# Kernel optimization log

Measured on AMD Instinct MI355X. Metric: run time of the kernel, lower is better.

The kernel has to match this reference:

```python
import jax, jax.numpy as jnp
import numpy as np

GRID = 14  # encoded_image_size

def _grid_edge_index():
    # Exact replica of build_adjacency_matrix().nonzero(): 8-neighbor 14x14 grid.
    edges = []
    for r in range(GRID):
        for c in range(GRID):
            i = r * GRID + c
            for rr in range(max(0, r - 1), min(r + 2, GRID)):
                for cc in range(max(0, c - 1), min(c + 2, GRID)):
                    if rr == r and cc == c:
                        continue
                    edges.append((i, rr * GRID + cc))
    return np.asarray(edges, dtype=np.int64).T  # (2, 1404)


def setup_inputs() -> dict:
    key = jax.random.key(0)
    k1, k2, k3 = jax.random.split(key, 3)
    B, H, W, C, Hid = 128, 14, 14, 2048, 1024
    x = jax.random.normal(k1, (B, H, W, C), dtype=jnp.float32)
    edge_index = jnp.asarray(_grid_edge_index())
    W1 = jax.random.normal(k2, (C, Hid), dtype=jnp.float32) * (1.0 / np.sqrt(C))
    b1 = jnp.zeros((Hid,), jnp.float32)
    W2 = jax.random.normal(k3, (Hid, C), dtype=jnp.float32) * (1.0 / np.sqrt(Hid))
    b2 = jnp.zeros((C,), jnp.float32)
    return {"x": x, "edge_index": edge_index, "W1": W1, "b1": b1, "W2": W2, "b2": b2}


def _gcn_conv(h, W, b, src, dst, dinv):
    # PyG GCNConv: linear transform, symmetric deg-normalized (A+I) aggregation, bias.
    h = h @ W  # [N, out]
    norm = (dinv[src] * dinv[dst])[:, None]
    agg = jax.ops.segment_sum(h[src] * norm, dst, num_segments=h.shape[0])
    agg = agg + h * (dinv * dinv)[:, None]  # self-loop term, norm = 1/deg_i
    return agg + b


def reference(x, edge_index, W1, b1, W2, b2):
    B, H, Wd, C = x.shape
    N = B * H * Wd
    # Faithful to original: permute(0,3,1,2) then reshape(-1, C) (layout-scrambling).
    xf = jnp.transpose(x, (0, 3, 1, 2)).reshape(-1, C)  # [N, C]
    src, dst = edge_index[0], edge_index[1]
    # Degrees over ALL N nodes: self-loop (=1) everywhere + incoming grid edges
    # (only first 196 nodes have grid neighbors; rest are passthrough).
    deg = jnp.ones((N,), xf.dtype).at[dst].add(1.0)
    dinv = jax.lax.rsqrt(deg)
    h = jax.nn.relu(_gcn_conv(xf, W1, b1, src, dst, dinv))
    h = jax.nn.relu(_gcn_conv(h, W2, b2, src, dst, dinv))
    # reshape + permute(0,3,1,2) + permute(0,2,3,1) == identity back to NHWC.
    return h.reshape(B, H, Wd, C)
```

## Files before the change

### kernel.cpp

```cpp
#include <hip/hip_runtime.h>

typedef float  float4_t __attribute__((ext_vector_type(4)));
typedef __bf16 bf16x8   __attribute__((ext_vector_type(8)));

#define BM 256
#define BN 128
#define BK 64

#define GLD16(g, l)                                                        \
    __builtin_amdgcn_global_load_lds(                                      \
        (const __attribute__((address_space(1))) void*)(g),                \
        (__attribute__((address_space(3))) void*)(l), 16, 0, 0)

__global__ __launch_bounds__(256)
void transpose_x_kernel(const float* __restrict__ x, __bf16* __restrict__ A1)
{
    __shared__ float sm[32 * 221];
    const int b  = blockIdx.y;
    const int c0 = blockIdx.x * 32;
    const int t  = threadIdx.x;

    const float* xb = x + (size_t)b * 401408;
    const int c4 = (t & 7) * 4;
    const int p0 = t >> 3;
#pragma unroll
    for (int k = 0; k < 7; ++k) {
        int p = p0 + k * 32;
        if (p < 196) {
            float4_t v = *(const float4_t*)&xb[(size_t)p * 2048 + c0 + c4];
#pragma unroll
            for (int i = 0; i < 4; ++i)
                sm[(c4 + i) * 221 + p + (p >> 3)] = v[i];
        }
    }
    __syncthreads();

    __bf16* ab = A1 + (size_t)b * 401408 + (size_t)c0 * 196;
#pragma unroll
    for (int k = 0; k < 4; ++k) {
        int o8 = k * 256 + t;
        if (o8 < 784) {
            int o  = o8 * 8;
            int cc = o / 196;
            int pp = o - cc * 196;
            bf16x8 v;
#pragma unroll
            for (int i = 0; i < 8; ++i) {
                v[i] = (__bf16)sm[cc * 221 + pp + (pp >> 3)];
                if (++pp == 196) { pp = 0; ++cc; }
            }
            *(bf16x8*)(ab + o) = v;
        }
    }
}

__global__ void transpose_w_kernel(const float* __restrict__ W, __bf16* __restrict__ Wt,
                                   int K, int N)
{
    __shared__ float tile[32][33];
    const int kt = blockIdx.x * 32, nt = blockIdx.y * 32;
    const int tx = threadIdx.x, ty = threadIdx.y;
#pragma unroll
    for (int rr = 0; rr < 4; ++rr)
        tile[ty + rr * 8][tx] = W[(size_t)(kt + ty + rr * 8) * N + nt + tx];
    __syncthreads();
#pragma unroll
    for (int rr = 0; rr < 4; ++rr)
        Wt[(size_t)(nt + ty + rr * 8) * K + kt + tx] = (__bf16)tile[tx][ty + rr * 8];
}

template<bool OUT_BF16, int LNX>
__global__ __launch_bounds__(512, 2)
void gemm_bt_kernel(const __bf16* __restrict__ A,
                    const __bf16* __restrict__ Bt,
                    const float* __restrict__ bias,
                    void* __restrict__ out,
                    float* __restrict__ raw_out,
                    int M, int N, int K)
{
    __shared__ __bf16 lds[3 * 24576];

    const int tid  = threadIdx.x;
    const int wid  = tid >> 6;
    const int lane = tid & 63;

    const int lid  = blockIdx.x + gridDim.x * blockIdx.y;
    const int xcd  = lid & 7;
    const int i0   = lid >> 3;
    const int ni   = i0 & ((1 << LNX) - 1);
    const int mseq = i0 >> LNX;
    const int mi   = (mseq << 3) + xcd;
    const int row0 = mi * BM;
    if (row0 >= M) return;
    const int col0 = ni * BN;

    const int wave_m = (wid >> 1) * 64;
    const int wave_n = (wid & 1) * 64;

    float4_t acc[4][4];
#pragma unroll
    for (int i = 0; i < 4; ++i)
#pragma unroll
        for (int j = 0; j < 4; ++j)
            acc[i][j] = (float4_t){0.f, 0.f, 0.f, 0.f};

    const int    srow  = (wid << 3) + (lane >> 3);
    const int    scol  = ((lane & 7) ^ (lane >> 3)) << 3;
    const int    wb    = wid << 9;
    const __bf16* gA   = A  + (size_t)(row0 + srow) * K + scol;
    const __bf16* gB   = Bt + (size_t)(col0 + srow) * K + scol;
    const size_t rstep = (size_t)64 * K;

#define STAGE_P1(t, da) do {                                   \
    const __bf16* ga = gA + (size_t)(t) * BK;                  \
    GLD16(ga,             (da) +         wb);                  \
    GLD16(ga +     rstep, (da) + 4096  + wb);                  \
    GLD16(ga + 2 * rstep, (da) + 8192  + wb);                  \
} while (0)
#define STAGE_P2(t, da) do {                                   \
    const __bf16* ga = gA + (size_t)(t) * BK + 3 * rstep;      \
    const __bf16* gb = gB + (size_t)(t) * BK;                  \
    GLD16(ga,             (da) + 12288 + wb);                  \
    GLD16(gb,             (da) + 16384 + wb);                  \
    GLD16(gb +     rstep, (da) + 20480 + wb);                  \
} while (0)

    STAGE_P1(0, lds);         STAGE_P2(0, lds);
    STAGE_P1(1, lds + 24576); STAGE_P2(1, lds + 24576);
    asm volatile("s_waitcnt vmcnt(6)" ::: "memory");
    __builtin_amdgcn_s_barrier();
    __builtin_amdgcn_sched_barrier(0);

    const int xorv = lane & 7;
    const int kq   = lane >> 4;
    const int swz0 = (kq ^ xorv) << 3;
    const int arow = (wave_m + (lane & 15)) * 64;
    const int brow = (wave_n + (lane & 15)) * 64;

    const int NTt = K / BK;
    int cur = 0, st2 = 2;
    for (int t = 0; t < NTt; ++t) {
        const __bf16* cA = lds + cur * 24576;
        const __bf16* cB = cA + 16384;
        __bf16* dst2 = lds + st2 * 24576;
        const bool do_stage = (t < NTt - 2);

        bf16x8 bfr[2][4], af0[2][2];
#pragma unroll
        for (int x = 0; x < 2; ++x) {
            const int sz = swz0 ^ (x << 5);
#pragma unroll
            for (int j = 0; j < 4; ++j)
                bfr[x][j] = *(const bf16x8*)&cB[brow + j * 1024 + sz];
#pragma unroll
            for (int i = 0; i < 2; ++i)
                af0[x][i] = *(const bf16x8*)&cA[arow + i * 1024 + sz];
        }
        if (do_stage) STAGE_P1(t + 2, dst2);
        __builtin_amdgcn_s_barrier();
        __builtin_amdgcn_sched_barrier(0);
        __builtin_amdgcn_s_setprio(1);
#pragma unroll
        for (int x = 0; x < 2; ++x)
#pragma unroll
            for (int i = 0; i < 2; ++i)
#pragma unroll
                for (int j = 0; j < 4; ++j)
                    acc[i][j] = __builtin_amdgcn_mfma_f32_16x16x32_bf16(
                        af0[x][i], bfr[x][j], acc[i][j], 0, 0, 0);
        __builtin_amdgcn_s_setprio(0);

        bf16x8 af1[2][2];
#pragma unroll
        for (int x = 0; x < 2; ++x) {
            const int sz = swz0 ^ (x << 5);
#pragma unroll
            for (int i = 0; i < 2; ++i)
                af1[x][i] = *(const bf16x8*)&cA[arow + (i + 2) * 1024 + sz];
        }
        if (do_stage) STAGE_P2(t + 2, dst2);
        if (t < NTt - 1) {
            asm volatile("s_waitcnt lgkmcnt(0)" ::: "memory");
            if (do_stage) asm volatile("s_waitcnt vmcnt(6)" ::: "memory");
            else          asm volatile("s_waitcnt vmcnt(0)" ::: "memory");
            __builtin_amdgcn_s_barrier();
            __builtin_amdgcn_sched_barrier(0);
        }
        __builtin_amdgcn_s_setprio(1);
#pragma unroll
        for (int x = 0; x < 2; ++x)
#pragma unroll
            for (int i = 0; i < 2; ++i)
#pragma unroll
                for (int j = 0; j < 4; ++j)
                    acc[i + 2][j] = __builtin_amdgcn_mfma_f32_16x16x32_bf16(
                        af1[x][i], bfr[x][j], acc[i + 2][j], 0, 0, 0);
        __builtin_amdgcn_s_setprio(0);

        cur = (cur == 2) ? 0 : cur + 1;
        st2 = (st2 == 2) ? 0 : st2 + 1;
    }
#undef STAGE_P1
#undef STAGE_P2

    const int crow = (lane >> 4) * 4;
    const int ccol = lane & 15;
    const bool has_raw = (row0 == 0);
#pragma unroll
    for (int i = 0; i < 4; ++i) {
#pragma unroll
        for (int j = 0; j < 4; ++j) {
            int gcol = col0 + wave_n + j * 16 + ccol;
            float bv = bias[gcol];
#pragma unroll
            for (int r = 0; r < 4; ++r) {
                int grow = row0 + wave_m + i * 16 + crow + r;
                float v = acc[i][j][r];
                if (has_raw && grow < 196) raw_out[grow * N + gcol] = v;
                float o = fmaxf(v + bv, 0.f);
                if (OUT_BF16) ((__bf16*)out)[(size_t)grow * N + gcol] = (__bf16)o;
                else          ((float*)out)[(size_t)grow * N + gcol] = o;
            }
        }
    }
}

template<typename OutT>
__global__ void fixup_kernel(const float* __restrict__ raw, const float* __restrict__ bias,
                             OutT* __restrict__ out, int N)
{
    const int q = blockIdx.x;
    const int r = q / 14, c = q % 14;
    int nbr[8];
    int cnt = 0;
    for (int rr = (r > 0 ? r - 1 : 0); rr <= (r < 13 ? r + 1 : 13); ++rr)
        for (int cc = (c > 0 ? c - 1 : 0); cc <= (c < 13 ? c + 1 : 13); ++cc)
            if (!(rr == r && cc == c)) nbr[cnt++] = rr * 14 + cc;
    const float dq    = 1.f / sqrtf(1.f + (float)cnt);
    const float wself = 1.f / (1.f + (float)cnt);
    float wn[8];
    for (int t = 0; t < cnt; ++t) {
        int pr = nbr[t] / 14, pc = nbr[t] % 14;
        int pcnt = ((pr < 13 ? pr + 1 : 13) - (pr > 0 ? pr - 1 : 0) + 1) *
                   ((pc < 13 ? pc + 1 : 13) - (pc > 0 ? pc - 1 : 0) + 1) - 1;
        wn[t] = dq / sqrtf(1.f + (float)pcnt);
    }
    const int ch = blockIdx.y * 256 + threadIdx.x;
    float s = raw[q * N + ch] * wself;
    for (int t = 0; t < cnt; ++t) s += raw[nbr[t] * N + ch] * wn[t];
    float o = fmaxf(s + bias[ch], 0.f);
    out[(size_t)q * N + ch] = (OutT)o;
}

extern "C" void kernel_launch(void* const* d_in, const int* in_sizes, int n_in,
                              void* d_out, int out_size, void* d_ws, size_t ws_size,
                              hipStream_t stream)
{
    const float* x  = (const float*)d_in[0];
    const float* W1 = (const float*)d_in[2];
    const float* b1 = (const float*)d_in[3];
    const float* W2 = (const float*)d_in[4];
    const float* b2 = (const float*)d_in[5];

    const int M = 25088, C = 2048, Hid = 1024;

    __bf16* A1 = (__bf16*)d_out;

    char* ws = (char*)d_ws;
    __bf16* A2    = (__bf16*)(ws);
    __bf16* W1t   = (__bf16*)(ws + 51380224);
    __bf16* W2t   = (__bf16*)(ws + 55574528);
    float*  h1raw = (float*)(ws + 59768832);
    float*  h2raw = (float*)(ws + 60571648);

    transpose_x_kernel<<<dim3(64, 128), 256, 0, stream>>>(x, A1);
    transpose_w_kernel<<<dim3(C / 32, Hid / 32), dim3(32, 8), 0, stream>>>(W1, W1t, C, Hid);
    transpose_w_kernel<<<dim3(Hid / 32, C / 32), dim3(32, 8), 0, stream>>>(W2, W2t, Hid, C);

    gemm_bt_kernel<true, 3><<<dim3(Hid / BN, 104), 512, 0, stream>>>(
        A1, W1t, b1, (void*)A2, h1raw, M, Hid, C);
    fixup_kernel<__bf16><<<dim3(196, Hid / 256), 256, 0, stream>>>(h1raw, b1, A2, Hid);

    gemm_bt_kernel<false, 4><<<dim3(C / BN, 104), 512, 0, stream>>>(
        A2, W2t, b2, d_out, h2raw, M, C, Hid);
    fixup_kernel<float><<<dim3(196, C / 256), 256, 0, stream>>>(h2raw, b2, (float*)d_out, C);
}
```

Baseline: 634.6 us.

## Use 4-wave GEMM blocks with 128x64 per-wave tiles and BK=32

The GEMM block shrinks from 8 waves to 4, so each wave now computes a 128x64 output tile with 32 accumulators, and the K step drops to 32 with a new LDS swizzle and staging layout. The aim is more MFMA work per LDS fragment load and less LDS traffic per FLOP, plus one barrier per K step instead of two. In exchange, register pressure roughly doubles, the halved K step means twice as many loop iterations and syncs, and each block has fewer waves to hide latency.

```diff
diff --git a/kernel.cpp b/kernel.cpp
--- a/kernel.cpp
+++ b/kernel.cpp
@@ -5,7 +5,7 @@
 
 #define BM 256
 #define BN 128
-#define BK 64
+#define BK 32
 
 #define GLD16(g, l)                                                        \
     __builtin_amdgcn_global_load_lds(                                      \
@@ -70,7 +70,7 @@
 }
 
 template<bool OUT_BF16, int LNX>
-__global__ __launch_bounds__(512, 2)
+__global__ __launch_bounds__(256, 2)
 void gemm_bt_kernel(const __bf16* __restrict__ A,
                     const __bf16* __restrict__ Bt,
                     const float* __restrict__ bias,
@@ -78,7 +78,7 @@
                     float* __restrict__ raw_out,
                     int M, int N, int K)
 {
-    __shared__ __bf16 lds[3 * 24576];
+    __shared__ __bf16 lds[3 * 12288];
 
     const int tid  = threadIdx.x;
     const int wid  = tid >> 6;
@@ -94,91 +94,69 @@
     if (row0 >= M) return;
     const int col0 = ni * BN;
 
-    const int wave_m = (wid >> 1) * 64;
+    const int wave_m = (wid >> 1) * 128;
     const int wave_n = (wid & 1) * 64;
 
-    float4_t acc[4][4];
-#pragma unroll
-    for (int i = 0; i < 4; ++i)
+    float4_t acc[8][4];
+#pragma unroll
+    for (int i = 0; i < 8; ++i)
 #pragma unroll
         for (int j = 0; j < 4; ++j)
             acc[i][j] = (float4_t){0.f, 0.f, 0.f, 0.f};
 
-    const int    srow  = (wid << 3) + (lane >> 3);
-    const int    scol  = ((lane & 7) ^ (lane >> 3)) << 3;
-    const int    wb    = wid << 9;
-    const __bf16* gA   = A  + (size_t)(row0 + srow) * K + scol;
-    const __bf16* gB   = Bt + (size_t)(col0 + srow) * K + scol;
-    const size_t rstep = (size_t)64 * K;
-
-#define STAGE_P1(t, da) do {                                   \
+    const int    S       = (lane & 7) ^ (lane >> 3);
+    const int    stg_row = (wid << 4) + ((lane >> 3) << 1) + (S & 1);
+    const int    stg_k   = (S >> 1) << 3;
+    const int    wb      = wid << 9;
+    const __bf16* gA     = A  + (size_t)(row0 + stg_row) * K + stg_k;
+    const __bf16* gB     = Bt + (size_t)(col0 + stg_row) * K + stg_k;
+
+#define STAGE(t, d) do {                                       \
     const __bf16* ga = gA + (size_t)(t) * BK;                  \
-    GLD16(ga,             (da) +         wb);                  \
-    GLD16(ga +     rstep, (da) + 4096  + wb);                  \
-    GLD16(ga + 2 * rstep, (da) + 8192  + wb);                  \
+    const __bf16* gb = gB + (size_t)(t) * BK;                  \
+    GLD16(ga,                    (d) +         wb);            \
+    GLD16(ga +  64 * (size_t)K,  (d) + 2048  + wb);            \
+    GLD16(ga + 128 * (size_t)K,  (d) + 4096  + wb);            \
+    GLD16(ga + 192 * (size_t)K,  (d) + 6144  + wb);            \
+    GLD16(gb,                    (d) + 8192  + wb);            \
+    GLD16(gb +  64 * (size_t)K,  (d) + 10240 + wb);            \
 } while (0)
-#define STAGE_P2(t, da) do {                                   \
-    const __bf16* ga = gA + (size_t)(t) * BK + 3 * rstep;      \
-    const __bf16* gb = gB + (size_t)(t) * BK;                  \
-    GLD16(ga,             (da) + 12288 + wb);                  \
-    GLD16(gb,             (da) + 16384 + wb);                  \
-    GLD16(gb +     rstep, (da) + 20480 + wb);                  \
-} while (0)
-
-    STAGE_P1(0, lds);         STAGE_P2(0, lds);
-    STAGE_P1(1, lds + 24576); STAGE_P2(1, lds + 24576);
+
+    STAGE(0, lds);
+    STAGE(1, lds + 12288);
     asm volatile("s_waitcnt vmcnt(6)" ::: "memory");
     __builtin_amdgcn_s_barrier();
     __builtin_amdgcn_sched_barrier(0);
 
-    const int xorv = lane & 7;
-    const int kq   = lane >> 4;
-    const int swz0 = (kq ^ xorv) << 3;
-    const int arow = (wave_m + (lane & 15)) * 64;
-    const int brow = (wave_n + (lane & 15)) * 64;
+    const int slotf   = ((2 * (lane >> 4) + (lane & 1)) ^ ((lane & 15) >> 1));
+    const int la_base = ((wave_m >> 1) + ((lane & 15) >> 1)) * 64 + slotf * 8;
+    const int lb_base = 8192 + ((wave_n >> 1) + ((lane & 15) >> 1)) * 64 + slotf * 8;
 
     const int NTt = K / BK;
     int cur = 0, st2 = 2;
     for (int t = 0; t < NTt; ++t) {
-        const __bf16* cA = lds + cur * 24576;
-        const __bf16* cB = cA + 16384;
-        __bf16* dst2 = lds + st2 * 24576;
+        const __bf16* cA = lds + cur * 12288;
+        __bf16* dst = lds + st2 * 12288;
         const bool do_stage = (t < NTt - 2);
 
-        bf16x8 bfr[2][4], af0[2][2];
-#pragma unroll
-        for (int x = 0; x < 2; ++x) {
-            const int sz = swz0 ^ (x << 5);
+        bf16x8 af[8], bfr[4];
+#pragma unroll
+        for (int i = 0; i < 8; ++i)
+            af[i] = *(const bf16x8*)&cA[la_base + i * 512];
+#pragma unroll
+        for (int j = 0; j < 4; ++j)
+            bfr[j] = *(const bf16x8*)&cA[lb_base + j * 512];
+        if (do_stage) STAGE(t + 2, dst);
+
+        __builtin_amdgcn_s_setprio(1);
+#pragma unroll
+        for (int i = 0; i < 8; ++i)
 #pragma unroll
             for (int j = 0; j < 4; ++j)
-                bfr[x][j] = *(const bf16x8*)&cB[brow + j * 1024 + sz];
-#pragma unroll
-            for (int i = 0; i < 2; ++i)
-                af0[x][i] = *(const bf16x8*)&cA[arow + i * 1024 + sz];
-        }
-        if (do_stage) STAGE_P1(t + 2, dst2);
-        __builtin_amdgcn_s_barrier();
-        __builtin_amdgcn_sched_barrier(0);
-        __builtin_amdgcn_s_setprio(1);
-#pragma unroll
-        for (int x = 0; x < 2; ++x)
-#pragma unroll
-            for (int i = 0; i < 2; ++i)
-#pragma unroll
-                for (int j = 0; j < 4; ++j)
-                    acc[i][j] = __builtin_amdgcn_mfma_f32_16x16x32_bf16(
-                        af0[x][i], bfr[x][j], acc[i][j], 0, 0, 0);
+                acc[i][j] = __builtin_amdgcn_mfma_f32_16x16x32_bf16(
+                    af[i], bfr[j], acc[i][j], 0, 0, 0);
         __builtin_amdgcn_s_setprio(0);
 
-        bf16x8 af1[2][2];
-#pragma unroll
-        for (int x = 0; x < 2; ++x) {
-            const int sz = swz0 ^ (x << 5);
-#pragma unroll
-            for (int i = 0; i < 2; ++i)
-                af1[x][i] = *(const bf16x8*)&cA[arow + (i + 2) * 1024 + sz];
-        }
-        if (do_stage) STAGE_P2(t + 2, dst2);
         if (t < NTt - 1) {
             asm volatile("s_waitcnt lgkmcnt(0)" ::: "memory");
             if (do_stage) asm volatile("s_waitcnt vmcnt(6)" ::: "memory");
@@ -186,28 +164,16 @@
             __builtin_amdgcn_s_barrier();
             __builtin_amdgcn_sched_barrier(0);
         }
-        __builtin_amdgcn_s_setprio(1);
-#pragma unroll
-        for (int x = 0; x < 2; ++x)
-#pragma unroll
-            for (int i = 0; i < 2; ++i)
-#pragma unroll
-                for (int j = 0; j < 4; ++j)
-                    acc[i + 2][j] = __builtin_amdgcn_mfma_f32_16x16x32_bf16(
-                        af1[x][i], bfr[x][j], acc[i + 2][j], 0, 0, 0);
-        __builtin_amdgcn_s_setprio(0);
-
         cur = (cur == 2) ? 0 : cur + 1;
         st2 = (st2 == 2) ? 0 : st2 + 1;
     }
-#undef STAGE_P1
-#undef STAGE_P2
+#undef STAGE
 
     const int crow = (lane >> 4) * 4;
     const int ccol = lane & 15;
     const bool has_raw = (row0 == 0);
 #pragma unroll
-    for (int i = 0; i < 4; ++i) {
+    for (int i = 0; i < 8; ++i) {
 #pragma unroll
         for (int j = 0; j < 4; ++j) {
             int gcol = col0 + wave_n + j * 16 + ccol;
@@ -277,11 +243,11 @@
     transpose_w_kernel<<<dim3(C / 32, Hid / 32), dim3(32, 8), 0, stream>>>(W1, W1t, C, Hid);
     transpose_w_kernel<<<dim3(Hid / 32, C / 32), dim3(32, 8), 0, stream>>>(W2, W2t, Hid, C);
 
-    gemm_bt_kernel<true, 3><<<dim3(Hid / BN, 104), 512, 0, stream>>>(
+    gemm_bt_kernel<true, 3><<<dim3(Hid / BN, 104), 256, 0, stream>>>(
         A1, W1t, b1, (void*)A2, h1raw, M, Hid, C);
     fixup_kernel<__bf16><<<dim3(196, Hid / 256), 256, 0, stream>>>(h1raw, b1, A2, Hid);
 
-    gemm_bt_kernel<false, 4><<<dim3(C / BN, 104), 512, 0, stream>>>(
+    gemm_bt_kernel<false, 4><<<dim3(C / BN, 104), 256, 0, stream>>>(
         A2, W2t, b2, d_out, h2raw, M, C, Hid);
     fixup_kernel<float><<<dim3(196, C / 256), 256, 0, stream>>>(h2raw, b2, (float*)d_out, C);
 }
```

New measurement: 618.3 us. 2.6% less time.
